# Kernel tuning notes

Measured on AMD Instinct MI355X. Metric: run time of the kernel, lower is better.

The kernel has to match this reference:

```python
import jax, jax.numpy as jnp
import numpy as np

G, N_PER, H, F_IN, E = 512, 128, 128, 133, 524288
K1, K2, K3 = 103, 83, 67  # ceil(0.8*n) chain: 128->103->83->67 (PyG TopKPooling ratio=0.8)
NEG = 0.01   # leaky_relu default slope
EPS = 1e-5   # BatchNorm eps


def setup_inputs() -> dict:
    key = jax.random.key(0)
    ks = jax.random.split(key, 16)
    e_per = E // G
    # edges are intra-graph: local endpoints + per-graph offset
    src_l = jax.random.randint(ks[0], (G, e_per), 0, N_PER)
    dst_l = jax.random.randint(ks[1], (G, e_per), 0, N_PER)
    off = (jnp.arange(G) * N_PER)[:, None]
    src = (src_l + off).reshape(-1).astype(jnp.int32)
    dst = (dst_l + off).reshape(-1).astype(jnp.int32)
    batch = jnp.repeat(jnp.arange(G, dtype=jnp.int32), N_PER)

    def rn(k, shape, scale=0.05):
        return jax.random.normal(k, shape, dtype=jnp.float32) * scale

    return dict(
        x=jax.random.normal(ks[2], (G * N_PER, F_IN), dtype=jnp.float32),
        src=src, dst=dst, batch=batch,
        W1=rn(ks[3], (F_IN, H)), b1=jnp.zeros((H,), jnp.float32),
        W2=rn(ks[4], (H, H)), b2=jnp.zeros((H,), jnp.float32),
        W3=rn(ks[5], (H, H)), b3=jnp.zeros((H,), jnp.float32),
        p1=rn(ks[6], (H,), 0.1), p2=rn(ks[7], (H,), 0.1), p3=rn(ks[8], (H,), 0.1),
        lin1_W=rn(ks[9], (2 * H, 1024)), lin1_b=jnp.zeros((1024,), jnp.float32),
        lin2_W=rn(ks[10], (1024, 64)), lin2_b=jnp.zeros((64,), jnp.float32),
        lin3_W=rn(ks[11], (64, 2)), lin3_b=jnp.zeros((2,), jnp.float32),
        bn1_g=jnp.ones((1024,), jnp.float32), bn1_b=jnp.zeros((1024,), jnp.float32),
        bn1_rm=jnp.zeros((1024,), jnp.float32), bn1_rv=jnp.ones((1024,), jnp.float32),
        bn2_g=jnp.ones((64,), jnp.float32), bn2_b=jnp.zeros((64,), jnp.float32),
        bn2_rm=jnp.zeros((64,), jnp.float32), bn2_rv=jnp.ones((64,), jnp.float32),
    )


def _gcn(x, W, b, src, dst, em, n_nodes):
    # GCNConv with self-loops & symmetric norm; em masks edges removed by pooling.
    deg = jax.ops.segment_sum(em, dst, num_segments=n_nodes) + 1.0  # +1 self loop
    dis = jax.lax.rsqrt(deg)
    h = x @ W
    coef = dis[src] * dis[dst] * em                      # [E]
    agg = jax.ops.segment_sum(h[src] * coef[:, None], dst, num_segments=n_nodes)
    return agg + h * (1.0 / deg)[:, None] + b            # self-loop term: deg_i^-1 * h_i


def _topk(x, p, src, dst, em, n_per, k):
    # TopKPooling: score = x@p/||p||, keep top-k per graph, gate by tanh(score).
    g = x.shape[0] // n_per
    score = (x @ p) / jnp.linalg.norm(p)                 # [g*n_per]
    vals, idx = jax.lax.top_k(score.reshape(g, n_per), k)  # [g,k]
    xk = jnp.take_along_axis(x.reshape(g, n_per, -1), idx[:, :, None], axis=1)
    x_new = (xk * jnp.tanh(vals)[:, :, None]).reshape(g * k, -1)
    # remap surviving edges; drop (mask) edges touching removed nodes
    remap = jnp.full((g * n_per,), -1, jnp.int32)
    gperm = (jnp.arange(g, dtype=jnp.int32)[:, None] * n_per + idx.astype(jnp.int32)).reshape(-1)
    remap = remap.at[gperm].set(jnp.arange(g * k, dtype=jnp.int32))
    s2, d2 = remap[src], remap[dst]
    ok = (s2 >= 0) & (d2 >= 0)
    return x_new, jnp.where(ok, s2, 0), jnp.where(ok, d2, 0), em * ok.astype(em.dtype)


def _readout(x, g):
    xg = x.reshape(g, -1, x.shape[-1])
    return jnp.concatenate([xg.max(axis=1), xg.mean(axis=1)], axis=-1)  # [g, 2H]


def _lrelu(v):
    return jax.nn.leaky_relu(v, NEG)


def _bn(v, gam, bet, rm, rv):  # eval-mode BatchNorm1d (running stats)
    return (v - rm) * jax.lax.rsqrt(rv + EPS) * gam + bet


def _forward(x, src, dst, W1, b1, W2, b2, W3, b3, p1, p2, p3,
             lin1_W, lin1_b, lin2_W, lin2_b, lin3_W, lin3_b,
             bn1_g, bn1_b, bn1_rm, bn1_rv, bn2_g, bn2_b, bn2_rm, bn2_rv):
    em = jnp.ones(src.shape, jnp.float32)
    h = _lrelu(_gcn(x, W1, b1, src, dst, em, G * N_PER))
    h, src, dst, em = _topk(h, p1, src, dst, em, N_PER, K1)
    r1 = _readout(h, G)
    h = _lrelu(_gcn(h, W2, b2, src, dst, em, G * K1))
    h, src, dst, em = _topk(h, p2, src, dst, em, K1, K2)
    r2 = _readout(h, G)
    h = _lrelu(_gcn(h, W3, b3, src, dst, em, G * K2))
    h, src, dst, em = _topk(h, p3, src, dst, em, K2, K3)
    r3 = _readout(h, G)
    z = r1 + r2 + r3                                      # [G, 2H]
    z = _bn(_lrelu(z @ lin1_W + lin1_b), bn1_g, bn1_b, bn1_rm, bn1_rv)
    z = _bn(_lrelu(z @ lin2_W + lin2_b), bn2_g, bn2_b, bn2_rm, bn2_rv)
    # dropout p=0.5 is identity in eval mode
    return z @ lin3_W + lin3_b                            # [G, num_classes]


def reference(x, src, dst, batch, W1, b1, W2, b2, W3, b3, p1, p2, p3,
              lin1_W, lin1_b, lin2_W, lin2_b, lin3_W, lin3_b,
              bn1_g, bn1_b, bn1_rm, bn1_rv, bn2_g, bn2_b, bn2_rm, bn2_rv):
    # batch is implicit in the regular [G, n_per] layout; kept for signature parity.
    return _forward(x, src, dst, W1, b1, W2, b2, W3, b3, p1, p2, p3,
                    lin1_W, lin1_b, lin2_W, lin2_b, lin3_W, lin3_b,
                    bn1_g, bn1_b, bn1_rm, bn1_rv, bn2_g, bn2_b, bn2_rm, bn2_rv)
```

## Files before the change

kernel.cpp:

```cpp
#include <hip/hip_runtime.h>

#define NEGS 0.01f
#define BNEPS 1e-5f

typedef short bf16x8 __attribute__((ext_vector_type(8)));
typedef float f32x4 __attribute__((ext_vector_type(4)));

__device__ __forceinline__ void split2(float v, short& hi, short& lo) {
    unsigned u = __float_as_uint(v);
    unsigned r = (u + 0x7FFFu + ((u >> 16) & 1u)) >> 16;
    hi = (short)r;
    float hf = __uint_as_float(r << 16);
    float l = v - hf;
    unsigned ul = __float_as_uint(l);
    lo = (short)((ul + 0x7FFFu + ((ul >> 16) & 1u)) >> 16);
}

__global__ __launch_bounds__(256) void split_all(
    const float* __restrict__ W1, const float* __restrict__ W2,
    const float* __restrict__ W3, const float* __restrict__ L1,
    short* __restrict__ h1, short* __restrict__ l1,
    short* __restrict__ h2, short* __restrict__ l2,
    short* __restrict__ h3, short* __restrict__ l3,
    short* __restrict__ h4, short* __restrict__ l4)
{
    int idx = blockIdx.x * 256 + threadIdx.x;
    const float* B; short *H, *L; int K, N, K32, loc;
    if (idx < 20480)      { B = W1; H = h1; L = l1; K = 133; N = 128;  K32 = 160; loc = idx; }
    else if (idx < 36864) { B = W2; H = h2; L = l2; K = 128; N = 128;  K32 = 128; loc = idx - 20480; }
    else if (idx < 53248) { B = W3; H = h3; L = l3; K = 128; N = 128;  K32 = 128; loc = idx - 36864; }
    else                  { B = L1; H = h4; L = l4; K = 256; N = 1024; K32 = 256; loc = idx - 53248; }
    int n = loc % N, k = loc / N;
    float v = (k < K) ? B[(long)k * N + n] : 0.f;
    short hi, lo; split2(v, hi, lo);
    H[(long)n * K32 + k] = hi;
    L[(long)n * K32 + k] = lo;
}

template<int K, int K32, int EPI>
__global__ __launch_bounds__(256) void gemm_bres(
    const float* __restrict__ A, const short* __restrict__ Bh_t,
    const short* __restrict__ Bl_t, float* __restrict__ C, int N,
    const float* __restrict__ bias, const float* __restrict__ bng,
    const float* __restrict__ bnb, const float* __restrict__ bnrm,
    const float* __restrict__ bnrv)
{
    constexpr int KP = K32 + 8;
    constexpr int NKS = K32 / 32;
    __shared__ short Bhs[128 * KP];
    __shared__ short Bls[128 * KP];

    const int tid = threadIdx.x;
    const int bm = blockIdx.x * 128, n0 = blockIdx.y * 128;
    const int lane = tid & 63, w = tid >> 6;
    const int lm = lane & 15, lk = (lane >> 4) * 8;

    for (int i = tid; i < 128 * (K32 / 8); i += 256) {
        int n = i / (K32 / 8), kb = (i % (K32 / 8)) * 8;
        *(bf16x8*)&Bhs[n * KP + kb] = *(const bf16x8*)&Bh_t[(long)(n0 + n) * K32 + kb];
        *(bf16x8*)&Bls[n * KP + kb] = *(const bf16x8*)&Bl_t[(long)(n0 + n) * K32 + kb];
    }
    __syncthreads();

    const f32x4 zz = {0.f, 0.f, 0.f, 0.f};
    f32x4 acc[2][8];
#pragma unroll
    for (int i = 0; i < 2; ++i)
#pragma unroll
        for (int j = 0; j < 8; ++j) acc[i][j] = zz;

    const int r0 = bm + w * 32;
    for (int ks = 0; ks < NKS; ++ks) {
        const int k0 = ks * 32 + lk;
        bf16x8 ah[2], al[2];
#pragma unroll
        for (int mt = 0; mt < 2; ++mt) {
            const long rowb = (long)(r0 + mt * 16 + lm) * K;
            float av[8];
            if constexpr (K % 4 == 0) {
                const float4 v0 = *(const float4*)&A[rowb + k0];
                const float4 v1 = *(const float4*)&A[rowb + k0 + 4];
                av[0] = v0.x; av[1] = v0.y; av[2] = v0.z; av[3] = v0.w;
                av[4] = v1.x; av[5] = v1.y; av[6] = v1.z; av[7] = v1.w;
            } else {
#pragma unroll
                for (int j = 0; j < 8; ++j) {
                    int kk = k0 + j;
                    av[j] = (kk < K) ? A[rowb + kk] : 0.f;
                }
            }
#pragma unroll
            for (int j = 0; j < 8; ++j) {
                short h_, l_; split2(av[j], h_, l_);
                ah[mt][j] = h_; al[mt][j] = l_;
            }
        }
#pragma unroll
        for (int nt = 0; nt < 8; ++nt) {
            bf16x8 bh = *(const bf16x8*)&Bhs[(nt * 16 + lm) * KP + k0];
            bf16x8 bl = *(const bf16x8*)&Bls[(nt * 16 + lm) * KP + k0];
#pragma unroll
            for (int mt = 0; mt < 2; ++mt) {
                acc[mt][nt] = __builtin_amdgcn_mfma_f32_16x16x32_bf16(ah[mt], bh, acc[mt][nt], 0, 0, 0);
                acc[mt][nt] = __builtin_amdgcn_mfma_f32_16x16x32_bf16(ah[mt], bl, acc[mt][nt], 0, 0, 0);
                acc[mt][nt] = __builtin_amdgcn_mfma_f32_16x16x32_bf16(al[mt], bh, acc[mt][nt], 0, 0, 0);
            }
        }
    }

#pragma unroll
    for (int mt = 0; mt < 2; ++mt) {
        const int row0 = r0 + mt * 16 + (lane >> 4) * 4;
#pragma unroll
        for (int nt = 0; nt < 8; ++nt) {
            const int col = n0 + nt * 16 + lm;
            float bi = 0.f, sc_ = 1.f, rm_ = 0.f, bb_ = 0.f;
            if constexpr (EPI == 1) {
                bi = bias[col];
                sc_ = (1.0f / sqrtf(bnrv[col] + BNEPS)) * bng[col];
                rm_ = bnrm[col]; bb_ = bnb[col];
            }
#pragma unroll
            for (int r = 0; r < 4; ++r) {
                float v = acc[mt][nt][r];
                if constexpr (EPI == 1) {
                    v += bi;
                    v = v >= 0.f ? v : NEGS * v;
                    v = (v - rm_) * sc_ + bb_;
                }
                C[(long)(row0 + r) * N + col] = v;
            }
        }
    }
}

template<int NC, int KK, bool FIRST, bool LAST, bool ACCUM>
__global__ __launch_bounds__(1024, 8) void gcn_topk(
    const float* __restrict__ h_pre,
    const int* __restrict__ srcIn, const int* __restrict__ dstIn,
    int* ePK,
    const float* __restrict__ bias, const float* __restrict__ p,
    float* __restrict__ x_new,
    float* __restrict__ z)
{
    __shared__ float h_s[NC][128];
    __shared__ float2 csr[1024];
    __shared__ int   head[NC];
    __shared__ float deg_s[NC], dis_s[NC], invd_s[NC];
    __shared__ float sc[128];
    __shared__ int   id[128];
    __shared__ float gate[KK];
    __shared__ float b_s[128], p_s[128];
    __shared__ int   remap_l[NC];
    __shared__ float pnorm;

    const int g = blockIdx.x, tid = threadIdx.x, lane = tid & 63;
    const int f4 = (tid & 31) * 4;
    const int grp = tid >> 5;
    const float NINF = -__builtin_inff();
    constexpr int NIT4 = (NC + 31) / 32;

    int es_r, ed_r; bool live;
    {
        int eg = g * 1024 + tid;
        if (FIRST) { es_r = srcIn[eg] & 127; ed_r = dstIn[eg] & 127; live = true; }
        else       { int pk = ePK[eg]; es_r = pk & 127; ed_r = (pk >> 7) & 127; live = (pk >> 14) != 0; }
    }

    {
        const float4* hp = (const float4*)(h_pre + (long)g * NC * 128);
        float4* h4 = (float4*)&h_s[0][0];
        for (int i = tid; i < NC * 32; i += 1024) h4[i] = hp[i];
    }
    if (tid < 128) { b_s[tid] = bias[tid]; p_s[tid] = p[tid]; }
    for (int i = tid; i < NC; i += 1024) { deg_s[i] = 1.f; head[i] = 0; }
    __syncthreads();

    if (tid < 64) {
        float s = p_s[tid] * p_s[tid] + p_s[tid + 64] * p_s[tid + 64];
#pragma unroll
        for (int o = 32; o; o >>= 1) s += __shfl_xor(s, o, 64);
        if (tid == 0) pnorm = sqrtf(s);
    }
    if (live) {
        atomicAdd(&deg_s[ed_r], 1.0f);
        atomicAdd(&head[ed_r], 1);
    }
    __syncthreads();

    for (int i = tid; i < NC; i += 1024) {
        float d = deg_s[i];
        dis_s[i] = 1.0f / sqrtf(d);
        invd_s[i] = 1.0f / d;
    }
    if (tid < 64) {
        int c0 = head[tid];
        int c1 = (tid + 64 < NC) ? head[tid + 64] : 0;
        int s0 = c0, s1 = c1;
#pragma unroll
        for (int o = 1; o < 64; o <<= 1) { int t = __shfl_up(s0, o, 64); if (lane >= o) s0 += t; }
        int tot0 = __shfl(s0, 63, 64);
#pragma unroll
        for (int o = 1; o < 64; o <<= 1) { int t = __shfl_up(s1, o, 64); if (lane >= o) s1 += t; }
        s1 += tot0;
        head[tid] = s0 - c0;
        if (tid + 64 < NC) head[tid + 64] = s1 - c1;
    }
    __syncthreads();

    if (live) {
        int slot = atomicAdd(&head[ed_r], 1);
        csr[slot] = make_float2(__int_as_float(es_r), dis_s[es_r] * dis_s[ed_r]);
    }
    __syncthreads();

    const float4 p4 = *(const float4*)&p_s[f4];
    const float4 b4 = *(const float4*)&b_s[f4];
    float4 va[NIT4];
#pragma unroll
    for (int i = 0; i < NIT4; ++i) {
        int nd = grp + i * 32;
        if ((NC & 31) == 0 || nd < NC) {
            int kb = nd ? head[nd - 1] : 0;
            int ke = head[nd];
            float4 acc = make_float4(0.f, 0.f, 0.f, 0.f);
            for (int k = kb; k < ke; ++k) {
                float2 rec = csr[k];
                const float4 hv = *(const float4*)&h_s[__float_as_int(rec.x)][f4];
                acc.x = fmaf(hv.x, rec.y, acc.x);
                acc.y = fmaf(hv.y, rec.y, acc.y);
                acc.z = fmaf(hv.z, rec.y, acc.z);
                acc.w = fmaf(hv.w, rec.y, acc.w);
            }
            const float4 h0 = *(const float4*)&h_s[nd][f4];
            const float iv = invd_s[nd];
            float4 v;
            v.x = acc.x + h0.x * iv + b4.x;
            v.y = acc.y + h0.y * iv + b4.y;
            v.z = acc.z + h0.z * iv + b4.z;
            v.w = acc.w + h0.w * iv + b4.w;
            v.x = v.x >= 0.f ? v.x : NEGS * v.x;
            v.y = v.y >= 0.f ? v.y : NEGS * v.y;
            v.z = v.z >= 0.f ? v.z : NEGS * v.z;
            v.w = v.w >= 0.f ? v.w : NEGS * v.w;
            va[i] = v;
            float ps = v.x * p4.x + v.y * p4.y + v.z * p4.z + v.w * p4.w;
            ps += __shfl_xor(ps, 16, 64);
            ps += __shfl_xor(ps, 8, 64);
            ps += __shfl_xor(ps, 4, 64);
            ps += __shfl_xor(ps, 2, 64);
            ps += __shfl_xor(ps, 1, 64);
            if ((tid & 31) == 0) sc[nd] = ps;
        }
    }
    __syncthreads();

#pragma unroll
    for (int i = 0; i < NIT4; ++i) {
        int nd = grp + i * 32;
        if ((NC & 31) == 0 || nd < NC) *(float4*)&h_s[nd][f4] = va[i];
    }
    __syncthreads();

    if (tid < 128) {
        if (tid < NC) { sc[tid] = sc[tid] / pnorm; id[tid] = tid; }
        else          { sc[tid] = NINF; id[tid] = 0x7fffffff; }
    }
    __syncthreads();

    if (tid < 64) {
        for (int size = 2; size <= 128; size <<= 1) {
            for (int stride = size >> 1; stride > 0; stride >>= 1) {
                int i = 2 * stride * (tid / stride) + (tid % stride);
                int j = i + stride;
                float si_ = sc[i], sj_ = sc[j];
                int ii = id[i], ij = id[j];
                bool iFirst = (si_ > sj_) || (si_ == sj_ && ii < ij);
                bool descRegion = ((i & size) == 0);
                bool doSwap = descRegion ? !iFirst : iFirst;
                if (doSwap) { sc[i] = sj_; sc[j] = si_; id[i] = ij; id[j] = ii; }
                __asm__ volatile("" ::: "memory");
            }
        }
    }
    __syncthreads();

    for (int j = tid; j < KK; j += 1024) gate[j] = tanhf(sc[j]);
    if constexpr (!LAST) {
        for (int i = tid; i < NC; i += 1024) remap_l[i] = -1;
    }
    __syncthreads();
    if constexpr (!LAST) {
        for (int j = tid; j < KK; j += 1024) remap_l[id[j]] = j;
    }
    __syncthreads();

    if constexpr (!LAST) {
        int s2 = remap_l[es_r], d2 = remap_l[ed_r];
        bool ok = (s2 >= 0) && (d2 >= 0);
        int lv = (live && ok) ? 1 : 0;
        ePK[g * 1024 + tid] = (ok ? s2 : 0) | ((ok ? d2 : 0) << 7) | (lv << 14);
    }

    {
        const int jj = tid >> 5;
        float4 rmx = make_float4(NINF, NINF, NINF, NINF);
        float4 rsm = make_float4(0.f, 0.f, 0.f, 0.f);
        for (int j = jj; j < KK; j += 32) {
            const float gt = gate[j];
            const float4 hv = *(const float4*)&h_s[id[j]][f4];
            float4 v;
            v.x = hv.x * gt; v.y = hv.y * gt; v.z = hv.z * gt; v.w = hv.w * gt;
            if constexpr (!LAST) *(float4*)&x_new[((long)g * KK + j) * 128 + f4] = v;
            rmx.x = fmaxf(rmx.x, v.x); rmx.y = fmaxf(rmx.y, v.y);
            rmx.z = fmaxf(rmx.z, v.z); rmx.w = fmaxf(rmx.w, v.w);
            rsm.x += v.x; rsm.y += v.y; rsm.z += v.z; rsm.w += v.w;
        }
        rmx.x = fmaxf(rmx.x, __shfl_xor(rmx.x, 32, 64));
        rmx.y = fmaxf(rmx.y, __shfl_xor(rmx.y, 32, 64));
        rmx.z = fmaxf(rmx.z, __shfl_xor(rmx.z, 32, 64));
        rmx.w = fmaxf(rmx.w, __shfl_xor(rmx.w, 32, 64));
        rsm.x += __shfl_xor(rsm.x, 32, 64);
        rsm.y += __shfl_xor(rsm.y, 32, 64);
        rsm.z += __shfl_xor(rsm.z, 32, 64);
        rsm.w += __shfl_xor(rsm.w, 32, 64);
        __syncthreads();
        if (lane < 32) {
            const int w = tid >> 6;
            *(float4*)&h_s[w][f4] = rmx;
            *(float4*)&h_s[16 + w][f4] = rsm;
        }
    }
    __syncthreads();

    if (tid < 128) {
        float m = h_s[0][tid], s = h_s[16][tid];
#pragma unroll
        for (int q = 1; q < 16; ++q) { m = fmaxf(m, h_s[q][tid]); s += h_s[16 + q][tid]; }
        float mean = s / (float)KK;
        if constexpr (ACCUM) {
            z[g * 256 + tid] += m;
            z[g * 256 + 128 + tid] += mean;
        } else {
            z[g * 256 + tid] = m;
            z[g * 256 + 128 + tid] = mean;
        }
    }
}

__global__ __launch_bounds__(256) void mlp_tail(
    const float* __restrict__ t1,
    const float* __restrict__ W2, const float* __restrict__ b2v,
    const float* __restrict__ g2, const float* __restrict__ bb2,
    const float* __restrict__ rm2, const float* __restrict__ rv2,
    const float* __restrict__ W3, const float* __restrict__ b3v,
    float* __restrict__ out)
{
    __shared__ float t1s[1024];
    __shared__ float part[4][64];
    __shared__ float t2s[64];
    const int row = blockIdx.x, tid = threadIdx.x;

    for (int i = tid; i < 1024; i += 256) t1s[i] = t1[(long)row * 1024 + i];
    __syncthreads();

    int c = tid & 63, seg = tid >> 6;
    float s = 0.f;
    for (int k = seg * 256; k < seg * 256 + 256; ++k)
        s = fmaf(t1s[k], W2[k * 64 + c], s);
    part[seg][c] = s;
    __syncthreads();

    if (tid < 64) {
        float v = part[0][c] + part[1][c] + part[2][c] + part[3][c] + b2v[c];
        v = v >= 0.f ? v : NEGS * v;
        v = (v - rm2[c]) * (1.0f / sqrtf(rv2[c] + BNEPS)) * g2[c] + bb2[c];
        t2s[c] = v;
    }
    __syncthreads();

    if (tid < 128) {
        int cc = tid >> 6, k = tid & 63;
        float prod = t2s[k] * W3[k * 2 + cc];
#pragma unroll
        for (int o = 32; o; o >>= 1) prod += __shfl_xor(prod, o, 64);
        if (k == 0) out[row * 2 + cc] = prod + b3v[cc];
    }
}

extern "C" void kernel_launch(void* const* d_in, const int* in_sizes, int n_in,
                              void* d_out, int out_size, void* d_ws, size_t ws_size,
                              hipStream_t stream)
{
    const float* x    = (const float*)d_in[0];
    const int*   src  = (const int*)d_in[1];
    const int*   dst  = (const int*)d_in[2];
    const float* W1   = (const float*)d_in[4];
    const float* b1   = (const float*)d_in[5];
    const float* W2   = (const float*)d_in[6];
    const float* b2   = (const float*)d_in[7];
    const float* W3   = (const float*)d_in[8];
    const float* b3   = (const float*)d_in[9];
    const float* p1   = (const float*)d_in[10];
    const float* p2   = (const float*)d_in[11];
    const float* p3   = (const float*)d_in[12];
    const float* l1W  = (const float*)d_in[13];
    const float* l1b  = (const float*)d_in[14];
    const float* l2W  = (const float*)d_in[15];
    const float* l2b  = (const float*)d_in[16];
    const float* l3W  = (const float*)d_in[17];
    const float* l3b  = (const float*)d_in[18];
    const float* bn1g = (const float*)d_in[19];
    const float* bn1b = (const float*)d_in[20];
    const float* bn1rm= (const float*)d_in[21];
    const float* bn1rv= (const float*)d_in[22];
    const float* bn2g = (const float*)d_in[23];
    const float* bn2b = (const float*)d_in[24];
    const float* bn2rm= (const float*)d_in[25];
    const float* bn2rv= (const float*)d_in[26];
    float* out = (float*)d_out;

    float* ws = (float*)d_ws;
    size_t o = 0;
    float* h_pre = ws + o; o += 65536L * 128;
    float* x_cur = ws + o; o += 52736L * 128;
    float* z     = ws + o; o += 512L * 256;
    float* t1    = ws + o; o += 512L * 1024;
    int*   ePK   = (int*)(ws + o); o += 524288;
    short* sp = (short*)(ws + o);
    short* h1s = sp;
    short* l1s = h1s + 20480;
    short* h2s = l1s + 20480;
    short* l2s = h2s + 16384;
    short* h3s = l2s + 16384;
    short* l3s = h3s + 16384;
    short* h4s = l3s + 16384;
    short* l4s = h4s + 262144;

    split_all<<<1232, 256, 0, stream>>>(W1, W2, W3, l1W,
        h1s, l1s, h2s, l2s, h3s, l3s, h4s, l4s);

    gemm_bres<133,160,0><<<dim3(512,1), 256, 0, stream>>>(
        x, h1s, l1s, h_pre, 128, nullptr, nullptr, nullptr, nullptr, nullptr);
    gcn_topk<128,103,true,false,false><<<512, 1024, 0, stream>>>(
        h_pre, src, dst, ePK, b1, p1, x_cur, z);

    gemm_bres<128,128,0><<<dim3(412,1), 256, 0, stream>>>(
        x_cur, h2s, l2s, h_pre, 128, nullptr, nullptr, nullptr, nullptr, nullptr);
    gcn_topk<103,83,false,false,true><<<512, 1024, 0, stream>>>(
        h_pre, nullptr, nullptr, ePK, b2, p2, x_cur, z);

    gemm_bres<128,128,0><<<dim3(332,1), 256, 0, stream>>>(
        x_cur, h3s, l3s, h_pre, 128, nullptr, nullptr, nullptr, nullptr, nullptr);
    gcn_topk<83,67,false,true,true><<<512, 1024, 0, stream>>>(
        h_pre, nullptr, nullptr, ePK, b3, p3, nullptr, z);

    gemm_bres<256,256,1><<<dim3(4,8), 256, 0, stream>>>(
        z, h4s, l4s, t1, 1024, l1b, bn1g, bn1b, bn1rm, bn1rv);
    mlp_tail<<<512, 256, 0, stream>>>(
        t1, l2W, l2b, bn2g, bn2b, bn2rm, bn2rv, l3W, l3b, out);
}
```

Baseline: 262.9 us.

## Fuse next-layer GEMM into gcn_topk epilogue and drop standalone GEMMs

Each gcn_topk block now multiplies its pooled, gated node features by the next layer's weights using split-bf16 MFMA and writes the pre-activation directly. This removes two separate gemm_bres launches and the x_new round trip through global memory. The h_s row stride is padded to 132, and the readout reduction reuses the csr scratch buffer. The gemm_bres low-weight tile is also read from global instead of LDS to cut LDS use, which adds global traffic inside the MFMA loop.

```diff
diff --git a/kernel.cpp b/kernel.cpp
--- a/kernel.cpp
+++ b/kernel.cpp
@@ -1,4 +1,5 @@
 #include <hip/hip_runtime.h>
+#include <hip/hip_bf16.h>
 
 #define NEGS 0.01f
 #define BNEPS 1e-5f
@@ -7,13 +8,12 @@
 typedef float f32x4 __attribute__((ext_vector_type(4)));
 
 __device__ __forceinline__ void split2(float v, short& hi, short& lo) {
-    unsigned u = __float_as_uint(v);
-    unsigned r = (u + 0x7FFFu + ((u >> 16) & 1u)) >> 16;
-    hi = (short)r;
-    float hf = __uint_as_float(r << 16);
-    float l = v - hf;
-    unsigned ul = __float_as_uint(l);
-    lo = (short)((ul + 0x7FFFu + ((ul >> 16) & 1u)) >> 16);
+    __hip_bfloat16 bh = __float2bfloat16(v);
+    unsigned short hu = __builtin_bit_cast(unsigned short, bh);
+    hi = (short)hu;
+    float hf = __uint_as_float(((unsigned)hu) << 16);
+    __hip_bfloat16 bl = __float2bfloat16(v - hf);
+    lo = (short)__builtin_bit_cast(unsigned short, bl);
 }
 
 __global__ __launch_bounds__(256) void split_all(
@@ -48,7 +48,6 @@
     constexpr int KP = K32 + 8;
     constexpr int NKS = K32 / 32;
     __shared__ short Bhs[128 * KP];
-    __shared__ short Bls[128 * KP];
 
     const int tid = threadIdx.x;
     const int bm = blockIdx.x * 128, n0 = blockIdx.y * 128;
@@ -58,7 +57,6 @@
     for (int i = tid; i < 128 * (K32 / 8); i += 256) {
         int n = i / (K32 / 8), kb = (i % (K32 / 8)) * 8;
         *(bf16x8*)&Bhs[n * KP + kb] = *(const bf16x8*)&Bh_t[(long)(n0 + n) * K32 + kb];
-        *(bf16x8*)&Bls[n * KP + kb] = *(const bf16x8*)&Bl_t[(long)(n0 + n) * K32 + kb];
     }
     __syncthreads();
 
@@ -98,7 +96,7 @@
 #pragma unroll
         for (int nt = 0; nt < 8; ++nt) {
             bf16x8 bh = *(const bf16x8*)&Bhs[(nt * 16 + lm) * KP + k0];
-            bf16x8 bl = *(const bf16x8*)&Bls[(nt * 16 + lm) * KP + k0];
+            bf16x8 bl = *(const bf16x8*)&Bl_t[(long)(n0 + nt * 16 + lm) * K32 + k0];
 #pragma unroll
             for (int mt = 0; mt < 2; ++mt) {
                 acc[mt][nt] = __builtin_amdgcn_mfma_f32_16x16x32_bf16(ah[mt], bh, acc[mt][nt], 0, 0, 0);
@@ -134,22 +132,24 @@
     }
 }
 
-template<int NC, int KK, bool FIRST, bool LAST, bool ACCUM>
+template<int NC, int KK, int MT, bool FIRST, bool LAST, bool ACCUM>
 __global__ __launch_bounds__(1024, 8) void gcn_topk(
-    const float* __restrict__ h_pre,
+    const float* __restrict__ h_in,
     const int* __restrict__ srcIn, const int* __restrict__ dstIn,
     int* ePK,
     const float* __restrict__ bias, const float* __restrict__ p,
-    float* __restrict__ x_new,
+    const short* __restrict__ Whi, const short* __restrict__ Wlo,
+    float* __restrict__ h_out,
     float* __restrict__ z)
 {
-    __shared__ float h_s[NC][128];
+    constexpr int GP = (MT > 0) ? MT * 16 : KK;
+    __shared__ float h_s[NC][132];
     __shared__ float2 csr[1024];
     __shared__ int   head[NC];
     __shared__ float deg_s[NC], dis_s[NC], invd_s[NC];
     __shared__ float sc[128];
     __shared__ int   id[128];
-    __shared__ float gate[KK];
+    __shared__ float gate[GP];
     __shared__ float b_s[128], p_s[128];
     __shared__ int   remap_l[NC];
     __shared__ float pnorm;
@@ -168,9 +168,11 @@
     }
 
     {
-        const float4* hp = (const float4*)(h_pre + (long)g * NC * 128);
-        float4* h4 = (float4*)&h_s[0][0];
-        for (int i = tid; i < NC * 32; i += 1024) h4[i] = hp[i];
+        const float* hp = h_in + (long)g * NC * 128;
+        for (int i = tid; i < NC * 32; i += 1024) {
+            int row = i >> 5, c4 = (i & 31) << 2;
+            *(float4*)&h_s[row][c4] = *(const float4*)&hp[row * 128 + c4];
+        }
     }
     if (tid < 128) { b_s[tid] = bias[tid]; p_s[tid] = p[tid]; }
     for (int i = tid; i < NC; i += 1024) { deg_s[i] = 1.f; head[i] = 0; }
@@ -285,7 +287,7 @@
     }
     __syncthreads();
 
-    for (int j = tid; j < KK; j += 1024) gate[j] = tanhf(sc[j]);
+    for (int j = tid; j < GP; j += 1024) gate[j] = (j < KK) ? tanhf(sc[j]) : 0.f;
     if constexpr (!LAST) {
         for (int i = tid; i < NC; i += 1024) remap_l[i] = -1;
     }
@@ -302,6 +304,52 @@
         ePK[g * 1024 + tid] = (ok ? s2 : 0) | ((ok ? d2 : 0) << 7) | (lv << 14);
     }
 
+    if constexpr (MT > 0) {
+        const int w = tid >> 6;
+        const int mt = w & 7, ntg = w >> 3;
+        if (mt < MT) {
+            const int lm = lane & 15, lk = (lane >> 4) * 8;
+            const int j0 = mt * 16 + lm;
+            const int srow = id[j0];
+            const float gt = gate[j0];
+            const f32x4 zz = {0.f, 0.f, 0.f, 0.f};
+            f32x4 acc[4] = {zz, zz, zz, zz};
+#pragma unroll
+            for (int ks = 0; ks < 4; ++ks) {
+                const int k0 = ks * 32 + lk;
+                float av[8];
+                *(float4*)&av[0] = *(const float4*)&h_s[srow][k0];
+                *(float4*)&av[4] = *(const float4*)&h_s[srow][k0 + 4];
+                bf16x8 ah, al;
+#pragma unroll
+                for (int jj = 0; jj < 8; ++jj) {
+                    short h_, l_; split2(av[jj] * gt, h_, l_);
+                    ah[jj] = h_; al[jj] = l_;
+                }
+#pragma unroll
+                for (int nt = 0; nt < 4; ++nt) {
+                    const int ncol = (ntg * 4 + nt) * 16 + lm;
+                    bf16x8 bh = *(const bf16x8*)&Whi[(long)ncol * 128 + k0];
+                    bf16x8 bl = *(const bf16x8*)&Wlo[(long)ncol * 128 + k0];
+                    acc[nt] = __builtin_amdgcn_mfma_f32_16x16x32_bf16(ah, bh, acc[nt], 0, 0, 0);
+                    acc[nt] = __builtin_amdgcn_mfma_f32_16x16x32_bf16(ah, bl, acc[nt], 0, 0, 0);
+                    acc[nt] = __builtin_amdgcn_mfma_f32_16x16x32_bf16(al, bh, acc[nt], 0, 0, 0);
+                }
+            }
+            const int r0 = mt * 16 + (lane >> 4) * 4;
+#pragma unroll
+            for (int nt = 0; nt < 4; ++nt) {
+                const int col = (ntg * 4 + nt) * 16 + lm;
+#pragma unroll
+                for (int r = 0; r < 4; ++r) {
+                    const int j = r0 + r;
+                    if (j < KK) h_out[((long)g * KK + j) * 128 + col] = acc[nt][r];
+                }
+            }
+        }
+    }
+
+    float* csrF = (float*)&csr[0];
     {
         const int jj = tid >> 5;
         float4 rmx = make_float4(NINF, NINF, NINF, NINF);
@@ -311,7 +359,6 @@
             const float4 hv = *(const float4*)&h_s[id[j]][f4];
             float4 v;
             v.x = hv.x * gt; v.y = hv.y * gt; v.z = hv.z * gt; v.w = hv.w * gt;
-            if constexpr (!LAST) *(float4*)&x_new[((long)g * KK + j) * 128 + f4] = v;
             rmx.x = fmaxf(rmx.x, v.x); rmx.y = fmaxf(rmx.y, v.y);
             rmx.z = fmaxf(rmx.z, v.z); rmx.w = fmaxf(rmx.w, v.w);
             rsm.x += v.x; rsm.y += v.y; rsm.z += v.z; rsm.w += v.w;
@@ -325,25 +372,29 @@
         rsm.z += __shfl_xor(rsm.z, 32, 64);
         rsm.w += __shfl_xor(rsm.w, 32, 64);
         __syncthreads();
-        if (lane < 32) {
-            const int w = tid >> 6;
-            *(float4*)&h_s[w][f4] = rmx;
-            *(float4*)&h_s[16 + w][f4] = rsm;
-        }
-    }
-    __syncthreads();
-
-    if (tid < 128) {
-        float m = h_s[0][tid], s = h_s[16][tid];
-#pragma unroll
-        for (int q = 1; q < 16; ++q) { m = fmaxf(m, h_s[q][tid]); s += h_s[16 + q][tid]; }
-        float mean = s / (float)KK;
-        if constexpr (ACCUM) {
-            z[g * 256 + tid] += m;
-            z[g * 256 + 128 + tid] += mean;
-        } else {
-            z[g * 256 + tid] = m;
-            z[g * 256 + 128 + tid] = mean;
+        if (lane < 32) *(float4*)&csrF[(tid >> 6) * 128 + f4] = rmx;
+        __syncthreads();
+        float m = 0.f;
+        if (tid < 128) {
+            m = csrF[tid];
+#pragma unroll
+            for (int q = 1; q < 16; ++q) m = fmaxf(m, csrF[q * 128 + tid]);
+        }
+        __syncthreads();
+        if (lane < 32) *(float4*)&csrF[(tid >> 6) * 128 + f4] = rsm;
+        __syncthreads();
+        if (tid < 128) {
+            float s = csrF[tid];
+#pragma unroll
+            for (int q = 1; q < 16; ++q) s += csrF[q * 128 + tid];
+            float mean = s / (float)KK;
+            if constexpr (ACCUM) {
+                z[g * 256 + tid] += m;
+                z[g * 256 + 128 + tid] += mean;
+            } else {
+                z[g * 256 + tid] = m;
+                z[g * 256 + 128 + tid] = mean;
+            }
         }
     }
 }
@@ -422,11 +473,11 @@
 
     float* ws = (float*)d_ws;
     size_t o = 0;
-    float* h_pre = ws + o; o += 65536L * 128;
-    float* x_cur = ws + o; o += 52736L * 128;
-    float* z     = ws + o; o += 512L * 256;
-    float* t1    = ws + o; o += 512L * 1024;
-    int*   ePK   = (int*)(ws + o); o += 524288;
+    float* h1 = ws + o; o += 65536L * 128;
+    float* h2 = ws + o; o += 52736L * 128;
+    float* z  = ws + o; o += 512L * 256;
+    float* t1 = ws + o; o += 512L * 1024;
+    int*   ePK = (int*)(ws + o); o += 524288;
     short* sp = (short*)(ws + o);
     short* h1s = sp;
     short* l1s = h1s + 20480;
@@ -436,24 +487,22 @@
     short* l3s = h3s + 16384;
     short* h4s = l3s + 16384;
     short* l4s = h4s + 262144;
+    float* h3 = h1;
 
     split_all<<<1232, 256, 0, stream>>>(W1, W2, W3, l1W,
         h1s, l1s, h2s, l2s, h3s, l3s, h4s, l4s);
 
     gemm_bres<133,160,0><<<dim3(512,1), 256, 0, stream>>>(
-        x, h1s, l1s, h_pre, 128, nullptr, nullptr, nullptr, nullptr, nullptr);
-    gcn_topk<128,103,true,false,false><<<512, 1024, 0, stream>>>(
-        h_pre, src, dst, ePK, b1, p1, x_cur, z);
-
-    gemm_bres<128,128,0><<<dim3(412,1), 256, 0, stream>>>(
-        x_cur, h2s, l2s, h_pre, 128, nullptr, nullptr, nullptr, nullptr, nullptr);
-    gcn_topk<103,83,false,false,true><<<512, 1024, 0, stream>>>(
-        h_pre, nullptr, nullptr, ePK, b2, p2, x_cur, z);
-
-    gemm_bres<128,128,0><<<dim3(332,1), 256, 0, stream>>>(
-        x_cur, h3s, l3s, h_pre, 128, nullptr, nullptr, nullptr, nullptr, nullptr);
-    gcn_topk<83,67,false,true,true><<<512, 1024, 0, stream>>>(
-        h_pre, nullptr, nullptr, ePK, b3, p3, nullptr, z);
+        x, h1s, l1s, h1, 128, nullptr, nullptr, nullptr, nullptr, nullptr);
+
+    gcn_topk<128,103,7,true,false,false><<<512, 1024, 0, stream>>>(
+        h1, src, dst, ePK, b1, p1, h2s, l2s, h2, z);
+
+    gcn_topk<103,83,6,false,false,true><<<512, 1024, 0, stream>>>(
+        h2, nullptr, nullptr, ePK, b2, p2, h3s, l3s, h3, z);
+
+    gcn_topk<83,67,0,false,true,true><<<512, 1024, 0, stream>>>(
+        h3, nullptr, nullptr, ePK, b3, p3, nullptr, nullptr, nullptr, z);
 
     gemm_bres<256,256,1><<<dim3(4,8), 256, 0, stream>>>(
         z, h4s, l4s, t1, 1024, l1b, bn1g, bn1b, bn1rm, bn1rv);
```

Result: slower. 282.6 us (+7.5%).
